# Performance work log

Measured on AMD Instinct MI355X. Metric: run time of the kernel, lower is better.

The kernel has to match this reference:

```python
import jax, jax.numpy as jnp
import numpy as np

HID = 512
NHEADS = 8
HEAD_DIM = HID // NHEADS  # 64
L = 2048
B = 4
LQ = 128
SCALE = float(np.sqrt(HEAD_DIM))


def _xavier(k, shape):
    lim = float(np.sqrt(6.0 / (shape[0] + shape[1])))
    return jax.random.uniform(k, shape, jnp.float32, -lim, lim)


def setup_inputs() -> dict:
    key = jax.random.key(0)
    ks = jax.random.split(key, 9)
    query = jax.random.normal(ks[0], (L, B, HID), jnp.float32)
    key_t = jax.random.normal(ks[1], (L, B, HID), jnp.float32)
    value = jax.random.normal(ks[2], (L, B, HID), jnp.float32)
    # 1 = pad, 0 = valid (code adds (1-mask).log() to scores)
    key_padding_mask = jax.random.bernoulli(ks[3], 0.1, (B, L)).astype(jnp.float32)
    question_rel_emb = jax.random.normal(ks[4], (LQ, LQ, B, HID), jnp.float32) * 0.02
    Wq = _xavier(ks[5], (HID, HID))
    Wk = _xavier(ks[6], (HID, HID))
    Wv = _xavier(ks[7], (HID, HID))
    Wo = _xavier(ks[8], (HID, HID))
    return dict(query=query, key_t=key_t, value=value,
                key_padding_mask=key_padding_mask,
                question_rel_emb=question_rel_emb,
                Wq=Wq, Wk=Wk, Wv=Wv, Wo=Wo)


def reference(query, key_t, value, key_padding_mask, question_rel_emb, Wq, Wk, Wv, Wo):
    # head_reshape: [L,B,HID] -> [B*K, L, D] (b outer, k inner, matching torch view)
    def heads(x, W):
        y = x @ W.T                                   # [L,B,HID]
        return jnp.swapaxes(y.reshape(L, B * NHEADS, HEAD_DIM), 0, 1)

    q = heads(query, Wq)    # [BK,L,D]
    k = heads(key_t, Wk)
    v = heads(value, Wv)

    attn = jnp.einsum('nld,nmd->nlm', q, k)            # [BK,L,L]

    # question relative bias: proj_key over [Lq,Lq,B,HID] -> [BK,Lq,Lq,D]
    qr = question_rel_emb @ Wk.T
    qr = qr.reshape(LQ, LQ, B * NHEADS, HEAD_DIM).transpose(2, 0, 1, 3)
    bias = jnp.einsum('nijd,nid->nij', qr, q[:, -LQ:])  # [BK,Lq,Lq]
    attn = attn.at[:, -LQ:, -LQ:].add(bias)

    attn = attn / SCALE

    # padding mask: repeat_interleave over batch, add log(1-mask) per key column
    kpm = jnp.repeat(key_padding_mask, NHEADS, axis=0)  # [BK,L]
    attn = attn + jnp.log1p(-kpm)[:, None, :]

    attn = jax.nn.softmax(attn, axis=-1)
    out = jnp.einsum('nlm,nmd->nld', attn, v)           # [BK,L,D]
    out = jnp.swapaxes(out, 0, 1).reshape(L, B, HID) @ Wo.T
    return (out, attn)
```

## Files before the change

### kernel.cpp

```cpp
#include <hip/hip_runtime.h>
#include <hip/hip_bf16.h>


using short8   = __attribute__((ext_vector_type(8))) short;
using short4v  = __attribute__((ext_vector_type(4))) short;
using ushort4v = __attribute__((ext_vector_type(4))) unsigned short;
using f32x4    = __attribute__((ext_vector_type(4))) float;

#define L_T   2048
#define B_T   4
#define HID_T 512
#define HD_T  64
#define LQ_T  128
#define L0_T  1920

__device__ __forceinline__ float b2f(unsigned short u){
  return __uint_as_float(((unsigned int)u) << 16);
}
__device__ __forceinline__ unsigned short f2b(float f){
  unsigned int u = __float_as_uint(f);
  u += 0x7FFFu + ((u >> 16) & 1u);
  return (unsigned short)(u >> 16);
}
__device__ __forceinline__ f32x4 mfma16(short8 a, short8 b, f32x4 c){
  return __builtin_amdgcn_mfma_f32_16x16x32_bf16(a, b, c, 0, 0, 0);
}
#if __has_builtin(__builtin_amdgcn_mfma_f32_16x16x16bf16_1k)
__device__ __forceinline__ f32x4 mfma16k16(short4v a, short4v b, f32x4 c){
  return __builtin_amdgcn_mfma_f32_16x16x16bf16_1k(a, b, c, 0, 0, 0);
}
#else
__device__ __forceinline__ f32x4 mfma16k16(short4v a, short4v b, f32x4 c){
  f32x4 d;
  asm("v_mfma_f32_16x16x16_bf16 %0, %1, %2, %0"
      : "=v"(d) : "v"(a), "v"(b), "0"(c));
  return d;
}
#endif

__global__ __launch_bounds__(256) void k_splitX(const float* __restrict__ x,
                                                unsigned short* __restrict__ hi,
                                                unsigned short* __restrict__ lo)
{
  int chunk = blockIdx.x * 256 + threadIdx.x;
  int flatrow = chunk >> 7;
  int hpos = (chunk & 127) * 4;
  f32x4 v = ((const f32x4*)x)[chunk];
  ushort4v h4, l4;
  #pragma unroll
  for (int e = 0; e < 4; e++){
    unsigned short h = f2b(v[e]);
    h4[e] = h;
    l4[e] = f2b(v[e] - b2f(h));
  }
  size_t idx = ((size_t)((flatrow >> 4) * 16 + (hpos >> 5))) * 512
             + (((hpos & 31) >> 3) * 16 + (flatrow & 15)) * 8 + (hpos & 7);
  *(ushort4v*)(hi + idx) = h4;
  *(ushort4v*)(lo + idx) = l4;
}

__global__ __launch_bounds__(256) void k_splitW(const float* __restrict__ w0,
                                                const float* __restrict__ w1,
                                                const float* __restrict__ w2,
                                                const float* __restrict__ w3,
                                                unsigned short* __restrict__ hi,
                                                unsigned short* __restrict__ lo)
{
  int wid = blockIdx.y;
  const float* src = (wid == 0) ? w0 : (wid == 1) ? w1 : (wid == 2) ? w2 : w3;
  int chunk = blockIdx.x * 256 + threadIdx.x;
  int o = chunk >> 7;
  int hpos = (chunk & 127) * 4;
  f32x4 v = ((const f32x4*)src)[chunk];
  ushort4v h4, l4;
  #pragma unroll
  for (int e = 0; e < 4; e++){
    unsigned short h = f2b(v[e]);
    h4[e] = h;
    l4[e] = f2b(v[e] - b2f(h));
  }
  size_t idx = ((size_t)(wid * 512 + (o >> 4) * 16 + (hpos >> 5))) * 512
             + (((hpos & 31) >> 3) * 16 + (o & 15)) * 8 + (hpos & 7);
  *(ushort4v*)(hi + idx) = h4;
  *(ushort4v*)(lo + idx) = l4;
}

__global__ __launch_bounds__(256) void k_proj(const unsigned short* __restrict__ Xh,
                                              const unsigned short* __restrict__ Xl,
                                              const unsigned short* __restrict__ Wh,
                                              const unsigned short* __restrict__ Wl,
                                              unsigned short* __restrict__ ohi,
                                              unsigned short* __restrict__ olo,
                                              unsigned short* __restrict__ ovt,
                                              int mode)
{
  int wv = threadIdx.x >> 6, lane = threadIdx.x & 63;
  int tid = blockIdx.x * 4 + wv;
  int mt = tid >> 3, nt = tid & 7;
  int row0 = mt * 16, col0 = nt * 64;
  int lhi = lane >> 4, llo = lane & 15;
  const short* XH = (const short*)Xh;
  const short* XL = (const short*)Xl;
  const short* WH = (const short*)Wh;
  const short* WL = (const short*)Wl;
  f32x4 acc[4] = {{0,0,0,0},{0,0,0,0},{0,0,0,0},{0,0,0,0}};
  #pragma unroll 4
  for (int k0 = 0; k0 < 512; k0 += 32){
    int kk = k0 >> 5;
    size_t aidx = (size_t)(mt * 16 + kk) * 512 + lane * 8;
    short8 ah = *(const short8*)(XH + aidx);
    short8 al = *(const short8*)(XL + aidx);
    #pragma unroll
    for (int cb = 0; cb < 4; cb++){
      size_t bidx = (size_t)(((col0 >> 4) + cb) * 16 + kk) * 512 + lane * 8;
      short8 bh = *(const short8*)(WH + bidx);
      short8 bl = *(const short8*)(WL + bidx);
      acc[cb] = mfma16(ah, bh, acc[cb]);
      acc[cb] = mfma16(al, bh, acc[cb]);
      acc[cb] = mfma16(ah, bl, acc[cb]);
    }
  }
  #pragma unroll
  for (int cb = 0; cb < 4; cb++){
    #pragma unroll
    for (int r = 0; r < 4; r++){
      int row = row0 + lhi * 4 + r;
      int o   = col0 + cb * 16 + llo;
      int l = row >> 2, bb = row & 3;
      int n = bb * 8 + (o >> 6), d = o & 63;
      float v = acc[cb][r];
      if (mode == 0){
        size_t idx = ((size_t)(n * 128 + (l >> 4)) * 2 + (d >> 5)) * 512
                   + (((d & 31) >> 3) * 16 + (l & 15)) * 8 + (d & 7);
        unsigned short h = f2b(v);
        ohi[idx] = h;
        olo[idx] = f2b(v - b2f(h));
      } else {
        int m = l;
        size_t idx = (((size_t)(n * 128 + (m >> 4)) * 4) + (d >> 4)) * 256
                   + ((m & 15) >> 2) * 64 + (d & 15) * 4 + (m & 3);
        ovt[idx] = f2b(v);
      }
    }
  }
}

__global__ __launch_bounds__(256) void k_t(const unsigned short* __restrict__ qhi,
                                           const unsigned short* __restrict__ qlo,
                                           const float* __restrict__ Wk,
                                           float* __restrict__ tb)
{
  int n = blockIdx.z, i = blockIdx.y;
  int h = blockIdx.x * 256 + threadIdx.x;
  __shared__ float qv[64];
  if (threadIdx.x < 64){
    int d = threadIdx.x;
    int row = L0_T + i;
    size_t idx = ((size_t)(n * 128 + (row >> 4)) * 2 + (d >> 5)) * 512
               + (((d & 31) >> 3) * 16 + (row & 15)) * 8 + (d & 7);
    qv[d] = b2f(qhi[idx]) + b2f(qlo[idx]);
  }
  __syncthreads();
  int kh = n & 7;
  float acc = 0.f;
  #pragma unroll 8
  for (int d = 0; d < 64; d++)
    acc += qv[d] * Wk[(kh * 64 + d) * 512 + h];
  tb[((size_t)n * LQ_T + i) * 512 + h] = acc;
}

__global__ __launch_bounds__(256) void k_bias(const float* __restrict__ tb,
                                              const float* __restrict__ qrem,
                                              float* __restrict__ bias)
{
  int bb = blockIdx.x & 3, i = blockIdx.x >> 2;
  __shared__ float ts[8][512];
  for (int idx = threadIdx.x; idx < 4096; idx += 256){
    int kh = idx >> 9, h = idx & 511;
    ts[kh][h] = tb[((size_t)(bb * 8 + kh) * LQ_T + i) * 512 + h];
  }
  __syncthreads();
  int wv = threadIdx.x >> 6, lane = threadIdx.x & 63;
  for (int j = wv; j < 128; j += 4){
    const float* qr = qrem + (((size_t)i * LQ_T + j) * B_T + bb) * 512;
    f32x4 v0 = *(const f32x4*)(qr + lane * 4);
    f32x4 v1 = *(const f32x4*)(qr + 256 + lane * 4);
    float pl[8];
    #pragma unroll
    for (int kh = 0; kh < 8; kh++){
      f32x4 t0 = *(const f32x4*)&ts[kh][lane * 4];
      f32x4 t1 = *(const f32x4*)&ts[kh][256 + lane * 4];
      pl[kh] = v0[0]*t0[0] + v0[1]*t0[1] + v0[2]*t0[2] + v0[3]*t0[3]
             + v1[0]*t1[0] + v1[1]*t1[1] + v1[2]*t1[2] + v1[3]*t1[3];
    }
    #pragma unroll
    for (int kh = 0; kh < 8; kh++){
      float s = pl[kh];
      #pragma unroll
      for (int msk = 1; msk < 64; msk <<= 1) s += __shfl_xor(s, msk);
      pl[kh] = s;
    }
    if (lane == 0){
      #pragma unroll
      for (int kh = 0; kh < 8; kh++)
        bias[((size_t)(bb * 8 + kh) * LQ_T + i) * LQ_T + j] = pl[kh];
    }
  }
}

__global__ __launch_bounds__(1024, 4) void k_attn(
    const unsigned short* __restrict__ qhp, const unsigned short* __restrict__ qlp,
    const unsigned short* __restrict__ khp, const unsigned short* __restrict__ klp,
    const float* __restrict__ bias, const float* __restrict__ kpm,
    const unsigned short* __restrict__ vpk,
    float* __restrict__ attnF, float* __restrict__ outbk)
{
  __shared__ __attribute__((aligned(16))) float pf[16 * 1024];
  __shared__ float2 red2[16 * 16];
  const int w = threadIdx.x >> 6, lane = threadIdx.x & 63;
  const int lhi = lane >> 4, llo = lane & 15;

  for (int u = blockIdx.x; u < 4096; u += gridDim.x){
    const int n = u >> 7, rb = u & 127;
    const int row0 = rb * 16, bb = n >> 3;

    const short* QH = (const short*)qhp + ((size_t)(n * 128 + rb) * 2) * 512 + lane * 8;
    const short* QL = (const short*)qlp + ((size_t)(n * 128 + rb) * 2) * 512 + lane * 8;
    short8 qh0 = *(const short8*)(QH);
    short8 qh1 = *(const short8*)(QH + 512);
    short8 ql0 = *(const short8*)(QL);
    short8 ql1 = *(const short8*)(QL + 512);
    const short* KH = (const short*)khp + (size_t)n * 131072 + w * 1024 + lane * 8;
    const short* KL = (const short*)klp + (size_t)n * 131072 + w * 1024 + lane * 8;

    float sv[8][4];
    #pragma unroll
    for (int t = 0; t < 8; t++){
      f32x4 acc = {0.f, 0.f, 0.f, 0.f};
      short8 kh0v = *(const short8*)(KH + t * 16384);
      short8 kh1v = *(const short8*)(KH + t * 16384 + 512);
      short8 kl0v = *(const short8*)(KL + t * 16384);
      short8 kl1v = *(const short8*)(KL + t * 16384 + 512);
      acc = mfma16(kh0v, qh0, acc);
      acc = mfma16(kl0v, qh0, acc);
      acc = mfma16(kh0v, ql0, acc);
      acc = mfma16(kh1v, qh1, acc);
      acc = mfma16(kl1v, qh1, acc);
      acc = mfma16(kh1v, ql1, acc);
      if (t == 7 && rb >= 120 && w >= 8){
        int i  = row0 - L0_T + llo;
        int j0 = (w - 8) * 16 + lhi * 4;
        f32x4 bv = *(const f32x4*)(bias + ((size_t)(n * 128 + i)) * 128 + j0);
        acc += bv;
      }
      f32x4 mkv = *(const f32x4*)(kpm + bb * 2048 + (w + t * 16) * 16 + lhi * 4);
      #pragma unroll
      for (int r = 0; r < 4; r++)
        sv[t][r] = acc[r] * 0.125f + ((mkv[r] != 0.f) ? -__builtin_inff() : 0.f);
    }

    float pm = sv[0][0];
    #pragma unroll
    for (int t = 0; t < 8; t++)
      #pragma unroll
      for (int r = 0; r < 4; r++) pm = fmaxf(pm, sv[t][r]);
    pm = fmaxf(pm, __shfl_xor(pm, 16));
    pm = fmaxf(pm, __shfl_xor(pm, 32));
    float es = 0.f;
    #pragma unroll
    for (int t = 0; t < 8; t++)
      #pragma unroll
      for (int r = 0; r < 4; r++){
        float e = __expf(sv[t][r] - pm);
        sv[t][r] = e;
        es += e;
      }
    es += __shfl_xor(es, 16);
    es += __shfl_xor(es, 32);
    if (lane < 16) red2[w * 16 + llo] = make_float2(pm, es);
    asm volatile("s_waitcnt lgkmcnt(0)\n\ts_barrier" ::: "memory");

    float2 c0 = red2[(lhi * 4 + 0) * 16 + llo];
    float2 c1 = red2[(lhi * 4 + 1) * 16 + llo];
    float2 c2 = red2[(lhi * 4 + 2) * 16 + llo];
    float2 c3 = red2[(lhi * 4 + 3) * 16 + llo];
    float mg = fmaxf(fmaxf(c0.x, c1.x), fmaxf(c2.x, c3.x));
    mg = fmaxf(mg, __shfl_xor(mg, 16));
    mg = fmaxf(mg, __shfl_xor(mg, 32));
    float cg = c0.y * __expf(c0.x - mg) + c1.y * __expf(c1.x - mg)
             + c2.y * __expf(c2.x - mg) + c3.y * __expf(c3.x - mg);
    cg += __shfl_xor(cg, 16);
    cg += __shfl_xor(cg, 32);
    float fac = __expf(pm - mg) / cg;

    float* aRow = attnF + ((size_t)(n * L_T + row0 + llo)) * L_T;
    const short* VP = (const short*)vpk + (size_t)n * 131072 + w * 1024 + lane * 4;
    f32x4 pacc0 = {0,0,0,0}, pacc1 = {0,0,0,0}, pacc2 = {0,0,0,0}, pacc3 = {0,0,0,0};
    #pragma unroll
    for (int t = 0; t < 8; t++){
      f32x4 pv;
      #pragma unroll
      for (int r = 0; r < 4; r++) pv[r] = sv[t][r] * fac;
      __builtin_nontemporal_store(pv, (f32x4*)(aRow + (w + t * 16) * 16 + lhi * 4));
      short4v pb;
      #pragma unroll
      for (int r = 0; r < 4; r++) pb[r] = (short)f2b(pv[r]);
      pacc0 = mfma16k16(*(const short4v*)(VP + t * 16384 +   0), pb, pacc0);
      pacc1 = mfma16k16(*(const short4v*)(VP + t * 16384 + 256), pb, pacc1);
      pacc2 = mfma16k16(*(const short4v*)(VP + t * 16384 + 512), pb, pacc2);
      pacc3 = mfma16k16(*(const short4v*)(VP + t * 16384 + 768), pb, pacc3);
    }

    float* pfw = pf + w * 1024 + llo * 64;
    *(f32x4*)(pfw + (( 0 + lhi * 4 + llo * 4) & 63)) = pacc0;
    *(f32x4*)(pfw + ((16 + lhi * 4 + llo * 4) & 63)) = pacc1;
    *(f32x4*)(pfw + ((32 + lhi * 4 + llo * 4) & 63)) = pacc2;
    *(f32x4*)(pfw + ((48 + lhi * 4 + llo * 4) & 63)) = pacc3;
    asm volatile("s_waitcnt lgkmcnt(0)\n\ts_barrier" ::: "memory");
    {
      int q = w, d = lane;
      int slot = (d + q * 4) & 63;
      float s = 0.f;
      #pragma unroll
      for (int ww = 0; ww < 16; ww++) s += pf[ww * 1024 + q * 64 + slot];
      outbk[((size_t)(n * L_T + row0 + q)) * HD_T + d] = s;
    }
  }
}

__global__ __launch_bounds__(256) void k_final(const float* __restrict__ outbk,
                                               const unsigned short* __restrict__ Wh,
                                               const unsigned short* __restrict__ Wl,
                                               float* __restrict__ y)
{
  int wv = threadIdx.x >> 6, lane = threadIdx.x & 63;
  int tid = blockIdx.x * 4 + wv;
  int mt = tid >> 5, nt = tid & 31;
  int row0 = mt * 16, col0 = nt * 16;
  int lhi = lane >> 4, llo = lane & 15;
  int arow = row0 + llo;
  int l = arow >> 2, bb = arow & 3;
  const short* WHs = (const short*)Wh;
  const short* WLs = (const short*)Wl;
  f32x4 acc = {0.f, 0.f, 0.f, 0.f};
  for (int k0 = 0; k0 < 512; k0 += 32){
    int c = k0 + lhi * 8;
    const float* ap = outbk + ((size_t)(bb * 8 + (c >> 6)) * L_T + l) * HD_T + (c & 63);
    f32x4 a01 = *(const f32x4*)ap;
    f32x4 a23 = *(const f32x4*)(ap + 4);
    short8 ahi, alo;
    #pragma unroll
    for (int e = 0; e < 4; e++){
      unsigned short h0 = f2b(a01[e]);
      ahi[e] = (short)h0;  alo[e] = (short)f2b(a01[e] - b2f(h0));
      unsigned short h1 = f2b(a23[e]);
      ahi[e + 4] = (short)h1;  alo[e + 4] = (short)f2b(a23[e] - b2f(h1));
    }
    size_t bidx = (size_t)(nt * 16 + (k0 >> 5)) * 512 + lane * 8;
    short8 bh = *(const short8*)(WHs + bidx);
    short8 bl = *(const short8*)(WLs + bidx);
    acc = mfma16(ahi, bh, acc);
    acc = mfma16(alo, bh, acc);
    acc = mfma16(ahi, bl, acc);
  }
  #pragma unroll
  for (int r = 0; r < 4; r++)
    y[(size_t)(row0 + lhi * 4 + r) * 512 + col0 + llo] = acc[r];
}

extern "C" void kernel_launch(void* const* d_in, const int* in_sizes, int n_in,
                              void* d_out, int out_size, void* d_ws, size_t ws_size,
                              hipStream_t stream)
{
  const float* query = (const float*)d_in[0];
  const float* key_t = (const float*)d_in[1];
  const float* value = (const float*)d_in[2];
  const float* kpm   = (const float*)d_in[3];
  const float* qrem  = (const float*)d_in[4];
  const float* Wq    = (const float*)d_in[5];
  const float* Wk    = (const float*)d_in[6];
  const float* Wv    = (const float*)d_in[7];
  const float* Wo    = (const float*)d_in[8];

  float* outY  = (float*)d_out;
  float* attnF = outY + (size_t)L_T * B_T * HID_T;

  char* wp = (char*)d_ws;
  const size_t SZ8M = (size_t)32 * 2048 * 64 * 2;
  unsigned short* qhp = (unsigned short*)wp; wp += SZ8M;
  unsigned short* qlp = (unsigned short*)wp; wp += SZ8M;
  unsigned short* khp = (unsigned short*)wp; wp += SZ8M;
  unsigned short* klp = (unsigned short*)wp; wp += SZ8M;
  unsigned short* vpk = (unsigned short*)wp; wp += SZ8M;
  unsigned short* whA = (unsigned short*)wp; wp += (size_t)4 * 512 * 512 * 2;
  unsigned short* wlA = (unsigned short*)wp; wp += (size_t)4 * 512 * 512 * 2;
  unsigned short* xh  = (unsigned short*)wp; wp += SZ8M;
  unsigned short* xl  = (unsigned short*)wp; wp += SZ8M;
  float* tbuf  = (float*)wp; wp += (size_t)32 * 128 * 512 * 4;
  float* biasb = (float*)wp; wp += (size_t)32 * 128 * 128 * 4;
  float* outbk = (float*)xh;

  const size_t WSTEP = (size_t)512 * 512;

  k_splitW<<<dim3(256, 4), 256, 0, stream>>>(Wq, Wk, Wv, Wo, whA, wlA);
  k_splitX<<<4096, 256, 0, stream>>>(query, xh, xl);
  k_proj<<<1024, 256, 0, stream>>>(xh, xl, whA + 0 * WSTEP, wlA + 0 * WSTEP,
                                   qhp, qlp, nullptr, 0);
  k_splitX<<<4096, 256, 0, stream>>>(key_t, xh, xl);
  k_proj<<<1024, 256, 0, stream>>>(xh, xl, whA + 1 * WSTEP, wlA + 1 * WSTEP,
                                   khp, klp, nullptr, 0);
  k_splitX<<<4096, 256, 0, stream>>>(value, xh, xl);
  k_proj<<<1024, 256, 0, stream>>>(xh, xl, whA + 2 * WSTEP, wlA + 2 * WSTEP,
                                   nullptr, nullptr, vpk, 1);
  k_t<<<dim3(2, 128, 32), 256, 0, stream>>>(qhp, qlp, Wk, tbuf);
  k_bias<<<512, 256, 0, stream>>>(tbuf, qrem, biasb);
  k_attn<<<512, 1024, 0, stream>>>(qhp, qlp, khp, klp, biasb, kpm,
                                   vpk, attnF, outbk);
  k_final<<<4096, 256, 0, stream>>>(outbk, whA + 3 * WSTEP, wlA + 3 * WSTEP, outY);
}
```

Baseline: 563.0 us.

## Fuse input splitting into projections, merge bias kernels, add MFMA priority hints

The separate fp32-to-bf16 hi/lo split kernels are removed, and the conversion is done inline inside a single merged projection kernel that handles Q, K and V in one launch. The t and bias kernels are merged so the intermediate tbuf no longer round-trips through global memory. The attention loop is changed from a grid-stride loop to fixed 8 units per block, and s_setprio is placed around its MFMA sections. This cuts launches and global traffic, at the cost of redundant conversion of each A tile across the 8 column-tile waves and strided fp32 loads.

Result: slower. 1.041 ms (+84.9%).

```diff
diff --git a/kernel.cpp b/kernel.cpp
--- a/kernel.cpp
+++ b/kernel.cpp
@@ -37,27 +37,6 @@
   return d;
 }
 #endif
-
-__global__ __launch_bounds__(256) void k_splitX(const float* __restrict__ x,
-                                                unsigned short* __restrict__ hi,
-                                                unsigned short* __restrict__ lo)
-{
-  int chunk = blockIdx.x * 256 + threadIdx.x;
-  int flatrow = chunk >> 7;
-  int hpos = (chunk & 127) * 4;
-  f32x4 v = ((const f32x4*)x)[chunk];
-  ushort4v h4, l4;
-  #pragma unroll
-  for (int e = 0; e < 4; e++){
-    unsigned short h = f2b(v[e]);
-    h4[e] = h;
-    l4[e] = f2b(v[e] - b2f(h));
-  }
-  size_t idx = ((size_t)((flatrow >> 4) * 16 + (hpos >> 5))) * 512
-             + (((hpos & 31) >> 3) * 16 + (flatrow & 15)) * 8 + (hpos & 7);
-  *(ushort4v*)(hi + idx) = h4;
-  *(ushort4v*)(lo + idx) = l4;
-}
 
 __global__ __launch_bounds__(256) void k_splitW(const float* __restrict__ w0,
                                                 const float* __restrict__ w1,
@@ -85,31 +64,46 @@
   *(ushort4v*)(lo + idx) = l4;
 }
 
-__global__ __launch_bounds__(256) void k_proj(const unsigned short* __restrict__ Xh,
-                                              const unsigned short* __restrict__ Xl,
-                                              const unsigned short* __restrict__ Wh,
-                                              const unsigned short* __restrict__ Wl,
-                                              unsigned short* __restrict__ ohi,
-                                              unsigned short* __restrict__ olo,
-                                              unsigned short* __restrict__ ovt,
-                                              int mode)
-{
+__global__ __launch_bounds__(256) void k_proj3(const float* __restrict__ Xq,
+                                               const float* __restrict__ Xk,
+                                               const float* __restrict__ Xv,
+                                               const unsigned short* __restrict__ WhA,
+                                               const unsigned short* __restrict__ WlA,
+                                               unsigned short* __restrict__ qhp,
+                                               unsigned short* __restrict__ qlp,
+                                               unsigned short* __restrict__ khp,
+                                               unsigned short* __restrict__ klp,
+                                               unsigned short* __restrict__ vpk)
+{
+  int sel = blockIdx.x >> 10;
+  int bx  = blockIdx.x & 1023;
+  const float* X = (sel == 0) ? Xq : (sel == 1) ? Xk : Xv;
+  const short* WH = (const short*)WhA + (size_t)sel * 262144;
+  const short* WL = (const short*)WlA + (size_t)sel * 262144;
+  unsigned short* ohi = (sel == 0) ? qhp : khp;
+  unsigned short* olo = (sel == 0) ? qlp : klp;
+
   int wv = threadIdx.x >> 6, lane = threadIdx.x & 63;
-  int tid = blockIdx.x * 4 + wv;
+  int tid = bx * 4 + wv;
   int mt = tid >> 3, nt = tid & 7;
   int row0 = mt * 16, col0 = nt * 64;
   int lhi = lane >> 4, llo = lane & 15;
-  const short* XH = (const short*)Xh;
-  const short* XL = (const short*)Xl;
-  const short* WH = (const short*)Wh;
-  const short* WL = (const short*)Wl;
+  int arow = row0 + llo;
   f32x4 acc[4] = {{0,0,0,0},{0,0,0,0},{0,0,0,0},{0,0,0,0}};
   #pragma unroll 4
   for (int k0 = 0; k0 < 512; k0 += 32){
+    const float* ap = X + (size_t)arow * 512 + k0 + lhi * 8;
+    f32x4 a01 = *(const f32x4*)ap;
+    f32x4 a23 = *(const f32x4*)(ap + 4);
+    short8 ah, al;
+    #pragma unroll
+    for (int e = 0; e < 4; e++){
+      unsigned short h0 = f2b(a01[e]);
+      ah[e] = (short)h0;  al[e] = (short)f2b(a01[e] - b2f(h0));
+      unsigned short h1 = f2b(a23[e]);
+      ah[e + 4] = (short)h1;  al[e + 4] = (short)f2b(a23[e] - b2f(h1));
+    }
     int kk = k0 >> 5;
-    size_t aidx = (size_t)(mt * 16 + kk) * 512 + lane * 8;
-    short8 ah = *(const short8*)(XH + aidx);
-    short8 al = *(const short8*)(XL + aidx);
     #pragma unroll
     for (int cb = 0; cb < 4; cb++){
       size_t bidx = (size_t)(((col0 >> 4) + cb) * 16 + kk) * 512 + lane * 8;
@@ -129,7 +123,7 @@
       int l = row >> 2, bb = row & 3;
       int n = bb * 8 + (o >> 6), d = o & 63;
       float v = acc[cb][r];
-      if (mode == 0){
+      if (sel != 2){
         size_t idx = ((size_t)(n * 128 + (l >> 4)) * 2 + (d >> 5)) * 512
                    + (((d & 31) >> 3) * 16 + (l & 15)) * 8 + (d & 7);
         unsigned short h = f2b(v);
@@ -139,45 +133,45 @@
         int m = l;
         size_t idx = (((size_t)(n * 128 + (m >> 4)) * 4) + (d >> 4)) * 256
                    + ((m & 15) >> 2) * 64 + (d & 15) * 4 + (m & 3);
-        ovt[idx] = f2b(v);
+        vpk[idx] = f2b(v);
       }
     }
   }
 }
 
-__global__ __launch_bounds__(256) void k_t(const unsigned short* __restrict__ qhi,
-                                           const unsigned short* __restrict__ qlo,
-                                           const float* __restrict__ Wk,
-                                           float* __restrict__ tb)
-{
-  int n = blockIdx.z, i = blockIdx.y;
-  int h = blockIdx.x * 256 + threadIdx.x;
-  __shared__ float qv[64];
-  if (threadIdx.x < 64){
-    int d = threadIdx.x;
+__global__ __launch_bounds__(256) void k_tb(const unsigned short* __restrict__ qhp,
+                                            const unsigned short* __restrict__ qlp,
+                                            const float* __restrict__ Wk,
+                                            const float* __restrict__ qrem,
+                                            float* __restrict__ bias)
+{
+  int bb = blockIdx.x & 3, i = blockIdx.x >> 2;
+  __shared__ float qv[8][64];
+  __shared__ float ts[8][512];
+  for (int idx = threadIdx.x; idx < 512; idx += 256){
+    int kh = idx >> 6, d = idx & 63;
+    int n = bb * 8 + kh;
     int row = L0_T + i;
-    size_t idx = ((size_t)(n * 128 + (row >> 4)) * 2 + (d >> 5)) * 512
-               + (((d & 31) >> 3) * 16 + (row & 15)) * 8 + (d & 7);
-    qv[d] = b2f(qhi[idx]) + b2f(qlo[idx]);
+    size_t qidx = ((size_t)(n * 128 + (row >> 4)) * 2 + (d >> 5)) * 512
+                + (((d & 31) >> 3) * 16 + (row & 15)) * 8 + (d & 7);
+    qv[kh][d] = b2f(qhp[qidx]) + b2f(qlp[qidx]);
   }
   __syncthreads();
-  int kh = n & 7;
-  float acc = 0.f;
-  #pragma unroll 8
-  for (int d = 0; d < 64; d++)
-    acc += qv[d] * Wk[(kh * 64 + d) * 512 + h];
-  tb[((size_t)n * LQ_T + i) * 512 + h] = acc;
-}
-
-__global__ __launch_bounds__(256) void k_bias(const float* __restrict__ tb,
-                                              const float* __restrict__ qrem,
-                                              float* __restrict__ bias)
-{
-  int bb = blockIdx.x & 3, i = blockIdx.x >> 2;
-  __shared__ float ts[8][512];
-  for (int idx = threadIdx.x; idx < 4096; idx += 256){
-    int kh = idx >> 9, h = idx & 511;
-    ts[kh][h] = tb[((size_t)(bb * 8 + kh) * LQ_T + i) * 512 + h];
+  {
+    int kh = threadIdx.x >> 5, h0 = (threadIdx.x & 31) * 16;
+    f32x4 a0 = {0,0,0,0}, a1 = {0,0,0,0}, a2 = {0,0,0,0}, a3 = {0,0,0,0};
+    for (int d = 0; d < 64; d++){
+      float qd = qv[kh][d];
+      const float* wr = Wk + (size_t)(kh * 64 + d) * 512 + h0;
+      a0 += qd * *(const f32x4*)(wr);
+      a1 += qd * *(const f32x4*)(wr + 4);
+      a2 += qd * *(const f32x4*)(wr + 8);
+      a3 += qd * *(const f32x4*)(wr + 12);
+    }
+    *(f32x4*)&ts[kh][h0]      = a0;
+    *(f32x4*)&ts[kh][h0 + 4]  = a1;
+    *(f32x4*)&ts[kh][h0 + 8]  = a2;
+    *(f32x4*)&ts[kh][h0 + 12] = a3;
   }
   __syncthreads();
   int wv = threadIdx.x >> 6, lane = threadIdx.x & 63;
@@ -220,7 +214,8 @@
   const int w = threadIdx.x >> 6, lane = threadIdx.x & 63;
   const int lhi = lane >> 4, llo = lane & 15;
 
-  for (int u = blockIdx.x; u < 4096; u += gridDim.x){
+  for (int j = 0; j < 8; ++j){
+    const int u = blockIdx.x * 8 + j;
     const int n = u >> 7, rb = u & 127;
     const int row0 = rb * 16, bb = n >> 3;
 
@@ -234,6 +229,7 @@
     const short* KL = (const short*)klp + (size_t)n * 131072 + w * 1024 + lane * 8;
 
     float sv[8][4];
+    __builtin_amdgcn_s_setprio(1);
     #pragma unroll
     for (int t = 0; t < 8; t++){
       f32x4 acc = {0.f, 0.f, 0.f, 0.f};
@@ -258,6 +254,7 @@
       for (int r = 0; r < 4; r++)
         sv[t][r] = acc[r] * 0.125f + ((mkv[r] != 0.f) ? -__builtin_inff() : 0.f);
     }
+    __builtin_amdgcn_s_setprio(0);
 
     float pm = sv[0][0];
     #pragma unroll
@@ -296,6 +293,7 @@
     float* aRow = attnF + ((size_t)(n * L_T + row0 + llo)) * L_T;
     const short* VP = (const short*)vpk + (size_t)n * 131072 + w * 1024 + lane * 4;
     f32x4 pacc0 = {0,0,0,0}, pacc1 = {0,0,0,0}, pacc2 = {0,0,0,0}, pacc3 = {0,0,0,0};
+    __builtin_amdgcn_s_setprio(1);
     #pragma unroll
     for (int t = 0; t < 8; t++){
       f32x4 pv;
@@ -310,6 +308,7 @@
       pacc2 = mfma16k16(*(const short4v*)(VP + t * 16384 + 512), pb, pacc2);
       pacc3 = mfma16k16(*(const short4v*)(VP + t * 16384 + 768), pb, pacc3);
     }
+    __builtin_amdgcn_s_setprio(0);
 
     float* pfw = pf + w * 1024 + llo * 64;
     *(f32x4*)(pfw + (( 0 + lhi * 4 + llo * 4) & 63)) = pacc0;
@@ -394,26 +393,15 @@
   unsigned short* vpk = (unsigned short*)wp; wp += SZ8M;
   unsigned short* whA = (unsigned short*)wp; wp += (size_t)4 * 512 * 512 * 2;
   unsigned short* wlA = (unsigned short*)wp; wp += (size_t)4 * 512 * 512 * 2;
-  unsigned short* xh  = (unsigned short*)wp; wp += SZ8M;
-  unsigned short* xl  = (unsigned short*)wp; wp += SZ8M;
-  float* tbuf  = (float*)wp; wp += (size_t)32 * 128 * 512 * 4;
   float* biasb = (float*)wp; wp += (size_t)32 * 128 * 128 * 4;
-  float* outbk = (float*)xh;
+  float* outbk = (float*)wp; wp += (size_t)32 * 2048 * 64 * 4;
 
   const size_t WSTEP = (size_t)512 * 512;
 
   k_splitW<<<dim3(256, 4), 256, 0, stream>>>(Wq, Wk, Wv, Wo, whA, wlA);
-  k_splitX<<<4096, 256, 0, stream>>>(query, xh, xl);
-  k_proj<<<1024, 256, 0, stream>>>(xh, xl, whA + 0 * WSTEP, wlA + 0 * WSTEP,
-                                   qhp, qlp, nullptr, 0);
-  k_splitX<<<4096, 256, 0, stream>>>(key_t, xh, xl);
-  k_proj<<<1024, 256, 0, stream>>>(xh, xl, whA + 1 * WSTEP, wlA + 1 * WSTEP,
-                                   khp, klp, nullptr, 0);
-  k_splitX<<<4096, 256, 0, stream>>>(value, xh, xl);
-  k_proj<<<1024, 256, 0, stream>>>(xh, xl, whA + 2 * WSTEP, wlA + 2 * WSTEP,
-                                   nullptr, nullptr, vpk, 1);
-  k_t<<<dim3(2, 128, 32), 256, 0, stream>>>(qhp, qlp, Wk, tbuf);
-  k_bias<<<512, 256, 0, stream>>>(tbuf, qrem, biasb);
+  k_proj3<<<3072, 256, 0, stream>>>(query, key_t, value, whA, wlA,
+                                    qhp, qlp, khp, klp, vpk);
+  k_tb<<<512, 256, 0, stream>>>(qhp, qlp, Wk, qrem, biasb);
   k_attn<<<512, 1024, 0, stream>>>(qhp, qlp, khp, klp, biasb, kpm,
                                    vpk, attnF, outbk);
   k_final<<<4096, 256, 0, stream>>>(outbk, whA + 3 * WSTEP, wlA + 3 * WSTEP, outY);
```
